# Kernel optimization log

Hardware: AMD Instinct MI355X
Metric: run time of the kernel (lower is better)

Reference implementation:

```python
import jax, jax.numpy as jnp
import numpy as np

B, S, H = 1, 2048, 4096
NH, NKV, HD = 32, 8, 128
GROUP = NH // NKV  # 4
SCALE = 0.08838834764831845  # 1/sqrt(head_dim)
ROPE_BASE = 10000.0


def setup_inputs() -> dict:
    key = jax.random.key(0)
    k1, k2, k3 = jax.random.split(key, 3)
    hidden_states = jax.random.normal(k1, (B, S, H), jnp.float32)
    # c_attn: [H + 2*NKV*HD, H] = [6144, 4096]; c_proj: [H, H]
    w_attn = jax.random.normal(k2, (H + 2 * NKV * HD, H), jnp.float32) * 0.02
    w_proj = jax.random.normal(k3, (H, H), jnp.float32) * (0.02 / np.sqrt(2 * 32))
    # standard rotate-half RoPE tables, shape [S, HD]
    inv_freq = 1.0 / (ROPE_BASE ** (jnp.arange(0, HD, 2, dtype=jnp.float32) / HD))
    freqs = jnp.outer(jnp.arange(S, dtype=jnp.float32), inv_freq)
    emb = jnp.concatenate([freqs, freqs], axis=-1)
    return {
        "hidden_states": hidden_states,
        "w_attn": w_attn,
        "w_proj": w_proj,
        "rope_cos": jnp.cos(emb),
        "rope_sin": jnp.sin(emb),
    }


def _apply_rope(x, cos, sin):
    # x: [B, heads, S, HD]; cos/sin: [S, HD] broadcast over batch/heads
    x1, x2 = jnp.split(x, 2, axis=-1)
    rot = jnp.concatenate([-x2, x1], axis=-1)
    return x * cos + rot * sin


def reference(hidden_states, w_attn, w_proj, rope_cos, rope_sin):
    b, s, _ = hidden_states.shape
    # fused QKV projection (no bias)
    qkv = hidden_states @ w_attn.T  # [B, S, H + 2*NKV*HD]
    qkv = qkv.reshape(b, s, NKV, (GROUP + 2) * HD)
    q = qkv[..., : GROUP * HD].reshape(b, s, NH, HD)
    k = qkv[..., GROUP * HD : (GROUP + 1) * HD]  # [B, S, NKV, HD]
    v = qkv[..., (GROUP + 1) * HD :]
    q = q.transpose(0, 2, 1, 3)  # [B, NH, S, HD]
    k = k.transpose(0, 2, 1, 3)  # [B, NKV, S, HD]
    v = v.transpose(0, 2, 1, 3)
    q = _apply_rope(q, rope_cos, rope_sin)
    k = _apply_rope(k, rope_cos, rope_sin)
    # GQA: group query heads per kv head instead of repeating K/V
    qg = q.reshape(b, NKV, GROUP, s, HD)
    scores = jnp.einsum("bkgqd,bksd->bkgqs", qg, k) * SCALE
    causal = jnp.tril(jnp.ones((s, s), dtype=bool))
    scores = jnp.where(causal, scores, jnp.finfo(scores.dtype).min)
    probs = jax.nn.softmax(scores, axis=-1)
    out = jnp.einsum("bkgqs,bksd->bkgqd", probs, v)
    out = out.reshape(b, NH, s, HD).transpose(0, 2, 1, 3).reshape(b, s, NH * HD)
    return out @ w_proj.T
```

## Files before the change

kernel.cpp:

```cpp
#include <hip/hip_runtime.h>
#include <cstdint>
#include <cstddef>

typedef __attribute__((ext_vector_type(4))) float f32x4;
typedef __attribute__((ext_vector_type(8))) short bf16x8;

#define S_LEN 2048
#define HDIM 4096
#define QKVD 6144
#define NHEAD 32
#define NKVH 8
#define HD 128
#define ATT_SCALE 0.08838834764831845f

__device__ __forceinline__ short f2bf(float f) {
  unsigned int u = __float_as_uint(f);
  u += 0x7FFFu + ((u >> 16) & 1u);
  return (short)(u >> 16);
}

__device__ __forceinline__ void gl_lds16(const short* g, short* l) {
  __builtin_amdgcn_global_load_lds((const __attribute__((address_space(1))) void*)g,
                                   (__attribute__((address_space(3))) void*)l,
                                   16, 0, 0);
}

template<int N> __device__ __forceinline__ void vmw() {
  if constexpr (N == 0) asm volatile("s_waitcnt vmcnt(0)" ::: "memory");
  else if constexpr (N == 1) asm volatile("s_waitcnt vmcnt(1)" ::: "memory");
  else if constexpr (N == 2) asm volatile("s_waitcnt vmcnt(2)" ::: "memory");
  else if constexpr (N == 3) asm volatile("s_waitcnt vmcnt(3)" ::: "memory");
  else if constexpr (N == 4) asm volatile("s_waitcnt vmcnt(4)" ::: "memory");
}

__global__ void cvt_kernel(const float* __restrict__ in, short* __restrict__ out, int n) {
  int i = (blockIdx.x * blockDim.x + threadIdx.x) * 4;
  if (i >= n) return;
  const float4 v = *reinterpret_cast<const float4*>(in + i);
  short4 o;
  o.x = f2bf(v.x); o.y = f2bf(v.y); o.z = f2bf(v.z); o.w = f2bf(v.w);
  *reinterpret_cast<short4*>(out + i) = o;
}

#define PHASEX(MH, NH, VM, STAGE) { \
    bf16x8 af[MQ][2], bfr[2][2]; \
    { const short* bA = lA + buf * ATILE; const short* bB = lB + buf * BTILE; \
      _Pragma("unroll") for (int m = 0; m < MQ; ++m) { \
        int row = wm * (BM >> 1) + (MH) * (BM >> 2) + m * 16 + l15; \
        _Pragma("unroll") for (int kk = 0; kk < 2; ++kk) { \
          int slot = ((kk << 2) + l4) ^ (row & 7); \
          af[m][kk] = *reinterpret_cast<const bf16x8*>(bA + row * 64 + slot * 8); } } \
      _Pragma("unroll") for (int n = 0; n < 2; ++n) { \
        int row = wn * 64 + (NH) * 32 + n * 16 + l15; \
        _Pragma("unroll") for (int kk = 0; kk < 2; ++kk) { \
          int slot = ((kk << 2) + l4) ^ (row & 7); \
          bfr[n][kk] = *reinterpret_cast<const bf16x8*>(bB + row * 64 + slot * 8); } } } \
    STAGE; \
    vmw<(VM)>(); \
    __builtin_amdgcn_s_barrier(); \
    __builtin_amdgcn_sched_barrier(0); \
    __builtin_amdgcn_s_setprio(1); \
    _Pragma("unroll") for (int m = 0; m < MQ; ++m) \
      _Pragma("unroll") for (int n = 0; n < 2; ++n) \
        _Pragma("unroll") for (int kk = 0; kk < 2; ++kk) \
          acc[(MH) * MQ + m][(NH) * 2 + n] = __builtin_amdgcn_mfma_f32_16x16x32_bf16( \
              af[m][kk], bfr[n][kk], acc[(MH) * MQ + m][(NH) * 2 + n], 0, 0, 0); \
    __builtin_amdgcn_s_setprio(0); }

template<int BM>
__global__ __launch_bounds__(512, 2) void gemm8p(const short* __restrict__ A,
                                                 const short* __restrict__ B,
                                                 float* __restrict__ C,
                                                 int M, int N, int K) {
  extern __shared__ short sm[];
  constexpr int MQ = BM / 64;
  constexpr int MR = BM / 32;
  constexpr int ATILE = BM * 64;
  constexpr int BTILE = 256 * 64;
  const int tid = threadIdx.x;
  const int wv = tid >> 6, lane = tid & 63;
  const int wm = wv >> 2, wn = wv & 3;
  const int l15 = lane & 15, l4 = lane >> 4;
  const int nbn = N >> 8;
  const int nwg = gridDim.x;
  const int bid = blockIdx.x;
  const int sbid = (bid & 7) * (nwg >> 3) + (bid >> 3);
  const int tm = (sbid / nbn) * BM, tn = (sbid % nbn) * 256;
  short* lA = sm;
  short* lB = sm + 2 * ATILE;
  (void)M;

  f32x4 acc[MR][4] = {};

  auto stageA = [&](int k0, int bufi, int sel) {
    short* dst = lA + bufi * ATILE;
#pragma unroll
    for (int j = 0; j < (BM == 256 ? 2 : 1); ++j) {
      int c = tid + j * 512;
      int blk = (BM == 256) ? (c >> 9) : (c >> 8);
      int rowoff = (BM == 256) ? ((c >> 3) & 63) : ((c >> 3) & 31);
      int slot = c & 7;
      int row = blk * (BM >> 1) + sel * (BM >> 2) + rowoff;
      gl_lds16(A + (size_t)(tm + row) * K + k0 + ((slot ^ (row & 7)) << 3),
               dst + row * 64 + slot * 8);
    }
  };
  auto stageB = [&](int k0, int bufi, int par) {
    short* dst = lB + bufi * BTILE;
#pragma unroll
    for (int j = 0; j < 2; ++j) {
      int c = tid + j * 512;
      int blk = c >> 8;
      int rowoff = (c >> 3) & 31;
      int slot = c & 7;
      int row = blk * 64 + par * 32 + rowoff;
      gl_lds16(B + (size_t)(tn + row) * K + k0 + ((slot ^ (row & 7)) << 3),
               dst + row * 64 + slot * 8);
    }
  };

  stageA(0, 0, 0);
  stageB(0, 0, 0);
  stageB(0, 0, 1);
  stageA(0, 0, 1);
  vmw<(BM == 256 ? 4 : 3)>();
  __builtin_amdgcn_s_barrier();
  __builtin_amdgcn_sched_barrier(0);

  const int KT = K >> 6;
  for (int t = 0; t < KT - 1; ++t) {
    const int buf = t & 1, nbuf = buf ^ 1, nk0 = (t + 1) << 6;
    PHASEX(0, 0, (BM == 256 ? 4 : 2), stageA(nk0, nbuf, 0))
    PHASEX(0, 1, (BM == 256 ? 4 : 3), stageB(nk0, nbuf, 0))
    PHASEX(1, 0, 99,                  stageB(nk0, nbuf, 1))
    PHASEX(1, 1, (BM == 256 ? 4 : 3), stageA(nk0, nbuf, 1))
  }
  {
    const int buf = (KT - 1) & 1;
    PHASEX(0, 0, (BM == 256 ? 2 : 1), (void)0)
    PHASEX(0, 1, 0,                   (void)0)
    PHASEX(1, 0, 99,                  (void)0)
    PHASEX(1, 1, 99,                  (void)0)
  }
#pragma unroll
  for (int m = 0; m < MR; ++m)
#pragma unroll
    for (int n = 0; n < 4; ++n)
#pragma unroll
      for (int r = 0; r < 4; ++r) {
        int row = tm + wm * (BM >> 1) + m * 16 + l4 * 4 + r;
        int col = tn + wn * 64 + n * 16 + l15;
        C[(size_t)row * N + col] = acc[m][n][r];
      }
}

__global__ void rope_kernel(const float* __restrict__ qkv,
                            const float* __restrict__ cb,
                            const float* __restrict__ sb,
                            short* __restrict__ Q,
                            short* __restrict__ Kx,
                            short* __restrict__ V) {
  int tid = blockIdx.x * blockDim.x + threadIdx.x;
  int s = tid / QKVD;
  int j = tid - s * QKVD;
  int g = j / 768;
  int idx = j - g * 768;
  float val = qkv[tid];
  if (idx < 640) {
    int part = idx >> 7;
    int d = idx & 127;
    int d2 = (d < 64) ? d + 64 : d - 64;
    float pv = qkv[(size_t)s * QKVD + g * 768 + part * 128 + d2];
    float c = cb[s * HD + d], sn = sb[s * HD + d];
    float ov = (d < 64) ? (val * c - pv * sn) : (val * c + pv * sn);
    if (part < 4) {
      int hh = g * 4 + part;
      Q[((size_t)hh * S_LEN + s) * HD + d] = f2bf(ov);
    } else {
      Kx[((size_t)g * S_LEN + s) * HD + d] = f2bf(ov);
    }
  } else {
    int d = idx - 640;
    V[((size_t)g * S_LEN + s) * HD + d] = f2bf(val);
  }
}

__global__ __launch_bounds__(256) void vtrans_kernel(const short* __restrict__ V,
                                                     short* __restrict__ Vt) {
  __shared__ short tile[64][72];
  const int kvh = blockIdx.z;
  const int s0 = blockIdx.x * 64, d0 = blockIdx.y * 64;
  const int t = threadIdx.x;
  const short* Vb = V + (size_t)kvh * S_LEN * HD;
  short* Vtb = Vt + (size_t)kvh * HD * S_LEN;
#pragma unroll
  for (int i = 0; i < 2; ++i) {
    int sl = i * 32 + (t >> 3), dl = (t & 7) * 8;
    bf16x8 v = *reinterpret_cast<const bf16x8*>(Vb + (size_t)(s0 + sl) * HD + d0 + dl);
    *reinterpret_cast<bf16x8*>(&tile[sl][dl]) = v;
  }
  __syncthreads();
#pragma unroll
  for (int i = 0; i < 2; ++i) {
    int dl = i * 32 + (t >> 3), sl = (t & 7) * 8;
    bf16x8 o;
#pragma unroll
    for (int j = 0; j < 8; ++j) o[j] = tile[sl + j][dl];
    *reinterpret_cast<bf16x8*>(Vtb + (size_t)(d0 + dl) * S_LEN + s0 + sl) = o;
  }
}

__global__ __launch_bounds__(256, 2) void attn_kernel(const short* __restrict__ Q,
                                                      const short* __restrict__ Kx,
                                                      const short* __restrict__ Vt,
                                                      short* __restrict__ AO) {
  __shared__ short lK[2 * 64 * 128];
  __shared__ unsigned int lPu[4 * 2 * 512];
  const int tt = threadIdx.x;
  const int w = tt >> 6, lane = tt & 63;
  const int l15 = lane & 15, l4 = lane >> 4;
  const int kvh = blockIdx.x;
  const int y = blockIdx.y;
  const int qt = (y < 32) ? (2 * y) : (127 - 2 * y);
  const int h = kvh * 4 + w;

  bf16x8 qf[2][4];
#pragma unroll
  for (int qa = 0; qa < 2; ++qa) {
    const short* qrow = Q + ((size_t)h * S_LEN + qt * 32 + qa * 16 + l15) * HD + l4 * 8;
#pragma unroll
    for (int fd = 0; fd < 4; ++fd)
      qf[qa][fd] = *reinterpret_cast<const bf16x8*>(qrow + fd * 32);
  }

  f32x4 o[2][8] = {};
  float m_run[2] = {-1e30f, -1e30f};
  float lsum[2] = {0.f, 0.f};

  const short* Kb = Kx + (size_t)kvh * S_LEN * HD;
  const short* Vb = Vt + (size_t)kvh * HD * S_LEN;
  const int nkt = (qt >> 1) + 1;

#pragma unroll
  for (int i = 0; i < 4; ++i) {
    int c = tt + i * 256, row = c >> 4, jj = (c & 15) ^ (row & 7);
    gl_lds16(Kb + (size_t)row * HD + jj * 8, lK + c * 8);
  }
  __syncthreads();

  int cur = 0;
  for (int kt = 0; kt < nkt; ++kt) {
    const int c0 = kt * 64;
    if (kt + 1 < nkt) {
      const short* Kg = Kb + (size_t)(c0 + 64) * HD;
      short* dst = lK + (cur ^ 1) * (64 * 128);
#pragma unroll
      for (int i = 0; i < 4; ++i) {
        int c = tt + i * 256, row = c >> 4, jj = (c & 15) ^ (row & 7);
        gl_lds16(Kg + (size_t)row * HD + jj * 8, dst + c * 8);
      }
    }
    const short* src = lK + cur * (64 * 128);
    f32x4 sf[2][4] = {};
    __builtin_amdgcn_s_setprio(1);
#pragma unroll
    for (int n = 0; n < 4; ++n) {
      bf16x8 kf[4];
#pragma unroll
      for (int fd = 0; fd < 4; ++fd) {
        int row = n * 16 + l15, jp = (l4 + fd * 4) ^ (l15 & 7);
        kf[fd] = *reinterpret_cast<const bf16x8*>(src + row * 128 + jp * 8);
      }
#pragma unroll
      for (int fd = 0; fd < 4; ++fd) {
        sf[0][n] = __builtin_amdgcn_mfma_f32_16x16x32_bf16(kf[fd], qf[0][fd], sf[0][n], 0, 0, 0);
        sf[1][n] = __builtin_amdgcn_mfma_f32_16x16x32_bf16(kf[fd], qf[1][fd], sf[1][n], 0, 0, 0);
      }
    }
    __builtin_amdgcn_s_setprio(0);
    bf16x8 vreg[8][2];
#pragma unroll
    for (int fd = 0; fd < 8; ++fd) {
      const short* vrow = Vb + (size_t)(fd * 16 + l15) * S_LEN + c0 + l4 * 8;
      vreg[fd][0] = *reinterpret_cast<const bf16x8*>(vrow);
      vreg[fd][1] = *reinterpret_cast<const bf16x8*>(vrow + 32);
    }
    const bool lastt = (kt == nkt - 1);
#pragma unroll
    for (int qa = 0; qa < 2; ++qa) {
      const int qrow_g = qt * 32 + qa * 16 + l15;
#pragma unroll
      for (int n = 0; n < 4; ++n)
#pragma unroll
        for (int r = 0; r < 4; ++r) {
          float v = sf[qa][n][r] * ATT_SCALE;
          if (lastt && (c0 + n * 16 + l4 * 4 + r) > qrow_g) v = -1e30f;
          sf[qa][n][r] = v;
        }
      float mx = sf[qa][0][0];
#pragma unroll
      for (int n = 0; n < 4; ++n)
#pragma unroll
        for (int r = 0; r < 4; ++r) mx = fmaxf(mx, sf[qa][n][r]);
      mx = fmaxf(mx, __shfl_xor(mx, 16, 64));
      mx = fmaxf(mx, __shfl_xor(mx, 32, 64));
      float mnew = fmaxf(m_run[qa], mx);
      float alpha = __expf(m_run[qa] - mnew);
      m_run[qa] = mnew;
      float ps = 0.f;
#pragma unroll
      for (int n = 0; n < 4; ++n)
#pragma unroll
        for (int r = 0; r < 4; ++r) {
          float e = __expf(sf[qa][n][r] - mnew);
          sf[qa][n][r] = e;
          ps += e;
        }
      lsum[qa] = lsum[qa] * alpha + ps;
#pragma unroll
      for (int n = 0; n < 4; ++n)
#pragma unroll
        for (int rp = 0; rp < 2; ++rp) {
          unsigned int pkv =
              ((unsigned int)(unsigned short)f2bf(sf[qa][n][rp * 2 + 1]) << 16) |
              (unsigned short)f2bf(sf[qa][n][rp * 2]);
          int kv5 = ((n & 1) << 4) + l4 * 4 + rp * 2;
          lPu[w * 1024 + qa * 512 + ((n >> 1) << 8) +
              (l15 + ((kv5 >> 3) << 4)) * 4 + ((kv5 & 7) >> 1)] = pkv;
        }
      float aO[4];
#pragma unroll
      for (int r = 0; r < 4; ++r) aO[r] = __shfl(alpha, l4 * 4 + r, 64);
#pragma unroll
      for (int fd = 0; fd < 8; ++fd) {
        o[qa][fd][0] *= aO[0]; o[qa][fd][1] *= aO[1];
        o[qa][fd][2] *= aO[2]; o[qa][fd][3] *= aO[3];
      }
    }
    asm volatile("s_waitcnt lgkmcnt(0)" ::: "memory");
    bf16x8 pf[2][2];
#pragma unroll
    for (int qa = 0; qa < 2; ++qa)
#pragma unroll
      for (int p = 0; p < 2; ++p)
        pf[qa][p] = *reinterpret_cast<const bf16x8*>(
            (const short*)lPu + (w * 1024 + qa * 512 + p * 256 + lane * 4) * 2);
    __builtin_amdgcn_s_setprio(1);
#pragma unroll
    for (int fd = 0; fd < 8; ++fd) {
      o[0][fd] = __builtin_amdgcn_mfma_f32_16x16x32_bf16(pf[0][0], vreg[fd][0], o[0][fd], 0, 0, 0);
      o[0][fd] = __builtin_amdgcn_mfma_f32_16x16x32_bf16(pf[0][1], vreg[fd][1], o[0][fd], 0, 0, 0);
      o[1][fd] = __builtin_amdgcn_mfma_f32_16x16x32_bf16(pf[1][0], vreg[fd][0], o[1][fd], 0, 0, 0);
      o[1][fd] = __builtin_amdgcn_mfma_f32_16x16x32_bf16(pf[1][1], vreg[fd][1], o[1][fd], 0, 0, 0);
    }
    __builtin_amdgcn_s_setprio(0);
    __syncthreads();
    cur ^= 1;
  }
#pragma unroll
  for (int qa = 0; qa < 2; ++qa) {
    float s = lsum[qa];
    s += __shfl_xor(s, 16, 64);
    s += __shfl_xor(s, 32, 64);
    float inv = 1.f / s;
    float iO[4];
#pragma unroll
    for (int r = 0; r < 4; ++r) iO[r] = __shfl(inv, l4 * 4 + r, 64);
#pragma unroll
    for (int fd = 0; fd < 8; ++fd)
#pragma unroll
      for (int r = 0; r < 4; ++r)
        AO[(size_t)(qt * 32 + qa * 16 + l4 * 4 + r) * HDIM + h * HD + fd * 16 + l15] =
            f2bf(o[qa][fd][r] * iO[r]);
  }
}

extern "C" void kernel_launch(void* const* d_in, const int* in_sizes, int n_in,
                              void* d_out, int out_size, void* d_ws, size_t ws_size,
                              hipStream_t stream) {
  const float* hidden = (const float*)d_in[0];
  const float* w_attn = (const float*)d_in[1];
  const float* w_proj = (const float*)d_in[2];
  const float* rcos = (const float*)d_in[3];
  const float* rsin = (const float*)d_in[4];
  float* out = (float*)d_out;
  char* ws = (char*)d_ws;

  short* Xb  = (short*)(ws);
  short* Wab = (short*)(ws + (16u << 20));
  short* Qb  = (short*)(ws + (16u << 20));
  short* Kb  = (short*)(ws + (32u << 20));
  short* Vb  = (short*)(ws + (36u << 20));
  short* Vtb = (short*)(ws + (40u << 20));
  float* QKVf = (float*)(ws + (64u << 20));
  short* Wpb = (short*)(ws + (64u << 20));
  short* AO  = Xb;

  const int nX = S_LEN * HDIM;
  const int nWa = QKVD * HDIM;
  const int nWp = HDIM * HDIM;

  hipFuncSetAttribute(reinterpret_cast<const void*>(gemm8p<256>),
                      hipFuncAttributeMaxDynamicSharedMemorySize, 131072);
  hipFuncSetAttribute(reinterpret_cast<const void*>(gemm8p<128>),
                      hipFuncAttributeMaxDynamicSharedMemorySize, 98304);

  cvt_kernel<<<nX / 1024, 256, 0, stream>>>(hidden, Xb, nX);
  cvt_kernel<<<nWa / 1024, 256, 0, stream>>>(w_attn, Wab, nWa);
  gemm8p<256><<<192, 512, 131072, stream>>>(Xb, Wab, QKVf, S_LEN, QKVD, HDIM);
  rope_kernel<<<(S_LEN * QKVD) / 256, 256, 0, stream>>>(QKVf, rcos, rsin, Qb, Kb, Vb);
  vtrans_kernel<<<dim3(S_LEN / 64, HD / 64, NKVH), 256, 0, stream>>>(Vb, Vtb);
  cvt_kernel<<<nWp / 1024, 256, 0, stream>>>(w_proj, Wpb, nWp);
  attn_kernel<<<dim3(NKVH, 64), 256, 0, stream>>>(Qb, Kb, Vtb, AO);
  gemm8p<128><<<256, 512, 98304, stream>>>(AO, Wpb, out, S_LEN, HDIM, HDIM);
}
```

Measured before the change: 366.5 us.

## Retile GEMM to fixed 128-row M with variable N, fuse V transpose into conversion

The GEMM template now fixes the M tile at 128 rows and parameterizes the N tile, so the QKV projection runs as 128x384 tiles over 256 workgroups instead of 256x256 over 192, which fills more CUs. The output projection moves from 128x256 to 128x256 under the new layout. RoPE now processes rotate-half pairs per thread and no longer writes V. The V transpose reads fp32 QKV directly and converts it to bf16, removing the intermediate V buffer and one pass over memory.

```diff
diff --git a/kernel.cpp b/kernel.cpp
--- a/kernel.cpp
+++ b/kernel.cpp
@@ -43,15 +43,15 @@
 }
 
 #define PHASEX(MH, NH, VM, STAGE) { \
-    bf16x8 af[MQ][2], bfr[2][2]; \
+    bf16x8 af[2][2], bfr[NQ][2]; \
     { const short* bA = lA + buf * ATILE; const short* bB = lB + buf * BTILE; \
-      _Pragma("unroll") for (int m = 0; m < MQ; ++m) { \
-        int row = wm * (BM >> 1) + (MH) * (BM >> 2) + m * 16 + l15; \
+      _Pragma("unroll") for (int m = 0; m < 2; ++m) { \
+        int row = wm * 64 + (MH) * 32 + m * 16 + l15; \
         _Pragma("unroll") for (int kk = 0; kk < 2; ++kk) { \
           int slot = ((kk << 2) + l4) ^ (row & 7); \
           af[m][kk] = *reinterpret_cast<const bf16x8*>(bA + row * 64 + slot * 8); } } \
-      _Pragma("unroll") for (int n = 0; n < 2; ++n) { \
-        int row = wn * 64 + (NH) * 32 + n * 16 + l15; \
+      _Pragma("unroll") for (int n = 0; n < NQ; ++n) { \
+        int row = wn * (BN >> 2) + n * 32 + (NH) * 16 + l15; \
         _Pragma("unroll") for (int kk = 0; kk < 2; ++kk) { \
           int slot = ((kk << 2) + l4) ^ (row & 7); \
           bfr[n][kk] = *reinterpret_cast<const bf16x8*>(bB + row * 64 + slot * 8); } } } \
@@ -60,60 +60,52 @@
     __builtin_amdgcn_s_barrier(); \
     __builtin_amdgcn_sched_barrier(0); \
     __builtin_amdgcn_s_setprio(1); \
-    _Pragma("unroll") for (int m = 0; m < MQ; ++m) \
-      _Pragma("unroll") for (int n = 0; n < 2; ++n) \
+    _Pragma("unroll") for (int m = 0; m < 2; ++m) \
+      _Pragma("unroll") for (int n = 0; n < NQ; ++n) \
         _Pragma("unroll") for (int kk = 0; kk < 2; ++kk) \
-          acc[(MH) * MQ + m][(NH) * 2 + n] = __builtin_amdgcn_mfma_f32_16x16x32_bf16( \
-              af[m][kk], bfr[n][kk], acc[(MH) * MQ + m][(NH) * 2 + n], 0, 0, 0); \
+          acc[(MH) * 2 + m][(NH) * NQ + n] = __builtin_amdgcn_mfma_f32_16x16x32_bf16( \
+              af[m][kk], bfr[n][kk], acc[(MH) * 2 + m][(NH) * NQ + n], 0, 0, 0); \
     __builtin_amdgcn_s_setprio(0); }
 
-template<int BM>
+template<int BN>
 __global__ __launch_bounds__(512, 2) void gemm8p(const short* __restrict__ A,
                                                  const short* __restrict__ B,
                                                  float* __restrict__ C,
                                                  int M, int N, int K) {
   extern __shared__ short sm[];
-  constexpr int MQ = BM / 64;
-  constexpr int MR = BM / 32;
-  constexpr int ATILE = BM * 64;
-  constexpr int BTILE = 256 * 64;
+  constexpr int NQ = BN / 128;
+  constexpr int ATILE = 128 * 64;
+  constexpr int BTILE = BN * 64;
   const int tid = threadIdx.x;
   const int wv = tid >> 6, lane = tid & 63;
   const int wm = wv >> 2, wn = wv & 3;
   const int l15 = lane & 15, l4 = lane >> 4;
-  const int nbn = N >> 8;
+  const int nbn = N / BN;
   const int nwg = gridDim.x;
   const int bid = blockIdx.x;
   const int sbid = (bid & 7) * (nwg >> 3) + (bid >> 3);
-  const int tm = (sbid / nbn) * BM, tn = (sbid % nbn) * 256;
+  const int tm = (sbid / nbn) * 128, tn = (sbid % nbn) * BN;
   short* lA = sm;
   short* lB = sm + 2 * ATILE;
   (void)M;
 
-  f32x4 acc[MR][4] = {};
+  f32x4 acc[4][2 * NQ] = {};
 
   auto stageA = [&](int k0, int bufi, int sel) {
     short* dst = lA + bufi * ATILE;
-#pragma unroll
-    for (int j = 0; j < (BM == 256 ? 2 : 1); ++j) {
-      int c = tid + j * 512;
-      int blk = (BM == 256) ? (c >> 9) : (c >> 8);
-      int rowoff = (BM == 256) ? ((c >> 3) & 63) : ((c >> 3) & 31);
-      int slot = c & 7;
-      int row = blk * (BM >> 1) + sel * (BM >> 2) + rowoff;
-      gl_lds16(A + (size_t)(tm + row) * K + k0 + ((slot ^ (row & 7)) << 3),
-               dst + row * 64 + slot * 8);
-    }
+    int rowIdx = tid >> 3;
+    int row = (rowIdx >> 5) * 64 + sel * 32 + (rowIdx & 31);
+    int slot = tid & 7;
+    gl_lds16(A + (size_t)(tm + row) * K + k0 + ((slot ^ (row & 7)) << 3),
+             dst + row * 64 + slot * 8);
   };
   auto stageB = [&](int k0, int bufi, int par) {
     short* dst = lB + bufi * BTILE;
 #pragma unroll
-    for (int j = 0; j < 2; ++j) {
-      int c = tid + j * 512;
-      int blk = c >> 8;
-      int rowoff = (c >> 3) & 31;
-      int slot = c & 7;
-      int row = blk * 64 + par * 32 + rowoff;
+    for (int j = 0; j < NQ; ++j) {
+      int rowIdx = (tid >> 3) + j * 64;
+      int row = (rowIdx >> 4) * 32 + par * 16 + (rowIdx & 15);
+      int slot = tid & 7;
       gl_lds16(B + (size_t)(tn + row) * K + k0 + ((slot ^ (row & 7)) << 3),
                dst + row * 64 + slot * 8);
     }
@@ -123,83 +115,79 @@
   stageB(0, 0, 0);
   stageB(0, 0, 1);
   stageA(0, 0, 1);
-  vmw<(BM == 256 ? 4 : 3)>();
+  vmw<NQ + 1>();
   __builtin_amdgcn_s_barrier();
   __builtin_amdgcn_sched_barrier(0);
 
   const int KT = K >> 6;
   for (int t = 0; t < KT - 1; ++t) {
     const int buf = t & 1, nbuf = buf ^ 1, nk0 = (t + 1) << 6;
-    PHASEX(0, 0, (BM == 256 ? 4 : 2), stageA(nk0, nbuf, 0))
-    PHASEX(0, 1, (BM == 256 ? 4 : 3), stageB(nk0, nbuf, 0))
-    PHASEX(1, 0, 99,                  stageB(nk0, nbuf, 1))
-    PHASEX(1, 1, (BM == 256 ? 4 : 3), stageA(nk0, nbuf, 1))
+    PHASEX(0, 0, 2,      stageA(nk0, nbuf, 0))
+    PHASEX(0, 1, NQ + 1, stageB(nk0, nbuf, 0))
+    PHASEX(1, 0, 99,     stageB(nk0, nbuf, 1))
+    PHASEX(1, 1, NQ + 1, stageA(nk0, nbuf, 1))
   }
   {
     const int buf = (KT - 1) & 1;
-    PHASEX(0, 0, (BM == 256 ? 2 : 1), (void)0)
-    PHASEX(0, 1, 0,                   (void)0)
-    PHASEX(1, 0, 99,                  (void)0)
-    PHASEX(1, 1, 99,                  (void)0)
-  }
-#pragma unroll
-  for (int m = 0; m < MR; ++m)
-#pragma unroll
-    for (int n = 0; n < 4; ++n)
-#pragma unroll
-      for (int r = 0; r < 4; ++r) {
-        int row = tm + wm * (BM >> 1) + m * 16 + l4 * 4 + r;
-        int col = tn + wn * 64 + n * 16 + l15;
-        C[(size_t)row * N + col] = acc[m][n][r];
-      }
-}
-
-__global__ void rope_kernel(const float* __restrict__ qkv,
-                            const float* __restrict__ cb,
-                            const float* __restrict__ sb,
-                            short* __restrict__ Q,
-                            short* __restrict__ Kx,
-                            short* __restrict__ V) {
+    PHASEX(0, 0, 1,  (void)0)
+    PHASEX(0, 1, 0,  (void)0)
+    PHASEX(1, 0, 99, (void)0)
+    PHASEX(1, 1, 99, (void)0)
+  }
+#pragma unroll
+  for (int mg = 0; mg < 4; ++mg)
+#pragma unroll
+    for (int NH = 0; NH < 2; ++NH)
+#pragma unroll
+      for (int n = 0; n < NQ; ++n)
+#pragma unroll
+        for (int r = 0; r < 4; ++r) {
+          int row = tm + wm * 64 + mg * 16 + l4 * 4 + r;
+          int col = tn + wn * (BN >> 2) + n * 32 + NH * 16 + l15;
+          C[(size_t)row * N + col] = acc[mg][NH * NQ + n][r];
+        }
+}
+
+__global__ void rope2_kernel(const float* __restrict__ qkv,
+                             const float* __restrict__ cb,
+                             const float* __restrict__ sb,
+                             short* __restrict__ Q,
+                             short* __restrict__ Kx) {
   int tid = blockIdx.x * blockDim.x + threadIdx.x;
-  int s = tid / QKVD;
-  int j = tid - s * QKVD;
-  int g = j / 768;
-  int idx = j - g * 768;
-  float val = qkv[tid];
-  if (idx < 640) {
-    int part = idx >> 7;
-    int d = idx & 127;
-    int d2 = (d < 64) ? d + 64 : d - 64;
-    float pv = qkv[(size_t)s * QKVD + g * 768 + part * 128 + d2];
-    float c = cb[s * HD + d], sn = sb[s * HD + d];
-    float ov = (d < 64) ? (val * c - pv * sn) : (val * c + pv * sn);
-    if (part < 4) {
-      int hh = g * 4 + part;
-      Q[((size_t)hh * S_LEN + s) * HD + d] = f2bf(ov);
-    } else {
-      Kx[((size_t)g * S_LEN + s) * HD + d] = f2bf(ov);
-    }
-  } else {
-    int d = idx - 640;
-    V[((size_t)g * S_LEN + s) * HD + d] = f2bf(val);
-  }
-}
-
-__global__ __launch_bounds__(256) void vtrans_kernel(const short* __restrict__ V,
-                                                     short* __restrict__ Vt) {
+  int dh = tid & 63;
+  int t2 = tid >> 6;
+  int part = t2 % 5;
+  int t3 = t2 / 5;
+  int g = t3 & 7;
+  int s = t3 >> 3;
+  const float* base = qkv + (size_t)s * QKVD + g * 768 + part * 128;
+  float v1 = base[dh], v2 = base[dh + 64];
+  float c = cb[s * HD + dh], sn = sb[s * HD + dh];
+  float o1 = v1 * c - v2 * sn;
+  float o2 = v2 * c + v1 * sn;
+  short* dst = (part < 4) ? (Q + ((size_t)(g * 4 + part) * S_LEN + s) * HD)
+                          : (Kx + ((size_t)g * S_LEN + s) * HD);
+  dst[dh] = f2bf(o1);
+  dst[dh + 64] = f2bf(o2);
+}
+
+__global__ __launch_bounds__(256) void vtrans2_kernel(const float* __restrict__ qkv,
+                                                      short* __restrict__ Vt) {
   __shared__ short tile[64][72];
   const int kvh = blockIdx.z;
   const int s0 = blockIdx.x * 64, d0 = blockIdx.y * 64;
   const int t = threadIdx.x;
-  const short* Vb = V + (size_t)kvh * S_LEN * HD;
+#pragma unroll
+  for (int i = 0; i < 4; ++i) {
+    int c = t + i * 256;
+    int sl = c >> 4, dl = (c & 15) * 4;
+    const float4 v = *reinterpret_cast<const float4*>(
+        qkv + (size_t)(s0 + sl) * QKVD + kvh * 768 + 640 + d0 + dl);
+    tile[sl][dl] = f2bf(v.x); tile[sl][dl + 1] = f2bf(v.y);
+    tile[sl][dl + 2] = f2bf(v.z); tile[sl][dl + 3] = f2bf(v.w);
+  }
+  __syncthreads();
   short* Vtb = Vt + (size_t)kvh * HD * S_LEN;
-#pragma unroll
-  for (int i = 0; i < 2; ++i) {
-    int sl = i * 32 + (t >> 3), dl = (t & 7) * 8;
-    bf16x8 v = *reinterpret_cast<const bf16x8*>(Vb + (size_t)(s0 + sl) * HD + d0 + dl);
-    *reinterpret_cast<bf16x8*>(&tile[sl][dl]) = v;
-  }
-  __syncthreads();
 #pragma unroll
   for (int i = 0; i < 2; ++i) {
     int dl = i * 32 + (t >> 3), sl = (t & 7) * 8;
@@ -390,7 +378,6 @@
   short* Wab = (short*)(ws + (16u << 20));
   short* Qb  = (short*)(ws + (16u << 20));
   short* Kb  = (short*)(ws + (32u << 20));
-  short* Vb  = (short*)(ws + (36u << 20));
   short* Vtb = (short*)(ws + (40u << 20));
   float* QKVf = (float*)(ws + (64u << 20));
   short* Wpb = (short*)(ws + (64u << 20));
@@ -400,17 +387,17 @@
   const int nWa = QKVD * HDIM;
   const int nWp = HDIM * HDIM;
 
+  hipFuncSetAttribute(reinterpret_cast<const void*>(gemm8p<384>),
+                      hipFuncAttributeMaxDynamicSharedMemorySize, 131072);
   hipFuncSetAttribute(reinterpret_cast<const void*>(gemm8p<256>),
-                      hipFuncAttributeMaxDynamicSharedMemorySize, 131072);
-  hipFuncSetAttribute(reinterpret_cast<const void*>(gemm8p<128>),
                       hipFuncAttributeMaxDynamicSharedMemorySize, 98304);
 
   cvt_kernel<<<nX / 1024, 256, 0, stream>>>(hidden, Xb, nX);
   cvt_kernel<<<nWa / 1024, 256, 0, stream>>>(w_attn, Wab, nWa);
-  gemm8p<256><<<192, 512, 131072, stream>>>(Xb, Wab, QKVf, S_LEN, QKVD, HDIM);
-  rope_kernel<<<(S_LEN * QKVD) / 256, 256, 0, stream>>>(QKVf, rcos, rsin, Qb, Kb, Vb);
-  vtrans_kernel<<<dim3(S_LEN / 64, HD / 64, NKVH), 256, 0, stream>>>(Vb, Vtb);
+  gemm8p<384><<<256, 512, 131072, stream>>>(Xb, Wab, QKVf, S_LEN, QKVD, HDIM);
+  rope2_kernel<<<(S_LEN * NKVH * 5 * 64) / 256, 256, 0, stream>>>(QKVf, rcos, rsin, Qb, Kb);
+  vtrans2_kernel<<<dim3(S_LEN / 64, HD / 64, NKVH), 256, 0, stream>>>(QKVf, Vtb);
   cvt_kernel<<<nWp / 1024, 256, 0, stream>>>(w_proj, Wpb, nWp);
   attn_kernel<<<dim3(NKVH, 64), 256, 0, stream>>>(Qb, Kb, Vtb, AO);
-  gemm8p<128><<<256, 512, 98304, stream>>>(AO, Wpb, out, S_LEN, HDIM, HDIM);
-}
+  gemm8p<256><<<256, 512, 98304, stream>>>(AO, Wpb, out, S_LEN, HDIM, HDIM);
+}
```

After: 353.0 us. 1.04x faster.
